# Optimization experiments

Measured on AMD Instinct MI355X. Metric: run time of the kernel, lower is better.

Reference implementation:

```python
import jax, jax.numpy as jnp
import numpy as np

H, DK, NHID, L, G = 8, 32, 256, 2, 16
SQRT_DK = float(np.sqrt(DK))
N_IN = (3, 3, 2)  # number of etypes whose dst is word, topic, doc (for mean cross-reducer)


def _seg_softmax_agg(a, val, dst, n):
    # per-destination-node softmax over incoming edges (DGL mailbox softmax), then weighted sum
    m = jax.ops.segment_max(a, dst, num_segments=n)
    m = jnp.where(m < -1e30, 0.0, m)  # empty segments
    ex = jnp.exp(a - m[dst])
    den = jax.ops.segment_sum(ex, dst, num_segments=n)
    w = ex / jnp.maximum(den, 1e-9)[dst]
    return jax.ops.segment_sum(w[..., None] * val, dst, num_segments=n)  # [n,H,DK]


def _forward(word_id, topic_id, g_word, g_topic, g_doc,
             src_ww, dst_ww, src_wd, dst_wd, src_wt, dst_wt, src_td, dst_td, src_tt, dst_tt,
             time_ww, time_wd, time_wt, time_td, y_data,
             word_embeds, topic_embeds, doc_gen, adapt_w, adapt_b,
             time_tab, time_w, time_b,
             kW, kB, qW, qB, vW, vB, aW, aB, skip, ln_g, ln_b,
             pri, attR, msgR, out_w, out_b):
    nd = g_doc.shape[0]
    # initial node features: word via adapt_ws, topic lookup, doc broadcast
    h = [word_embeds[word_id] @ adapt_w + adapt_b,
         topic_embeds[topic_id],
         jnp.tile(doc_gen, (nd, 1))]
    te = lambda t: time_tab[t] @ time_w + time_b  # RelTemporalEncoding: lin(emb(t)) -> [E, DK]
    th_ww, th_wd, th_wt, th_td = te(time_ww), te(time_wd), te(time_wt), te(time_td)
    # etype index order: wt, wd, td, tt, ww, tw, dt, dw ; ntype index: 0=word,1=topic,2=doc
    rels = [(0, 0, 1, src_wt, dst_wt, th_wt), (1, 0, 2, src_wd, dst_wd, th_wd),
            (2, 1, 2, src_td, dst_td, th_td), (3, 1, 1, src_tt, dst_tt, None),
            (4, 0, 0, src_ww, dst_ww, th_ww), (5, 1, 0, dst_wt, src_wt, th_wt),
            (6, 2, 1, dst_td, src_td, th_td), (7, 2, 0, dst_wd, src_wd, th_wd)]
    for li in range(L):
        k = [(h[i] @ kW[li, i] + kB[li, i]).reshape(-1, H, DK) for i in range(3)]
        q = [(h[i] @ qW[li, i] + qB[li, i]).reshape(-1, H, DK) for i in range(3)]
        v = [(h[i] @ vW[li, i] + vB[li, i]).reshape(-1, H, DK) for i in range(3)]
        t = [jnp.zeros((h[i].shape[0], NHID), h[i].dtype) for i in range(3)]
        for (e, s, d, src, dst, th) in rels:
            key = jnp.einsum('ehk,hkl->ehl', k[s][src], attR[li, e])
            a = (q[d][dst] * key).sum(-1) * pri[li, e] / SQRT_DK  # [E,H]
            val = jnp.einsum('ehk,hkl->ehl', v[s][src], msgR[li, e])
            if th is not None:
                val = val + th[:, None, :]  # temporal encoding broadcast over heads
            n = h[d].shape[0]
            he = _seg_softmax_agg(a, val, dst, n)
            t[d] = t[d] + jax.nn.relu(he.reshape(n, NHID))  # relu per etype, then mean
        nh = []
        for i in range(3):
            alpha = jax.nn.sigmoid(skip[li, i])
            trans = (t[i] / N_IN[i]) @ aW[li, i] + aB[li, i]
            out = trans * alpha + h[i] * (1.0 - alpha)
            mu = out.mean(-1, keepdims=True)
            var = ((out - mu) ** 2).mean(-1, keepdims=True)
            nh.append((out - mu) / jnp.sqrt(var + 1e-5) * ln_g[li, i] + ln_b[li, i])
        h = nh
    gmax = lambda x, g: jax.ops.segment_max(x, g, num_segments=G)  # dgl.max_nodes
    gi = jnp.concatenate([gmax(h[2], g_doc), gmax(h[0], g_word), gmax(h[1], g_topic)], -1)
    logits = gi @ out_w + out_b  # [G,1]
    z = logits.reshape(-1)
    loss = jnp.mean(jnp.maximum(z, 0.0) - z * y_data + jnp.log1p(jnp.exp(-jnp.abs(z))))
    return loss, jax.nn.sigmoid(logits)


def setup_inputs():
    key = jax.random.key(0)
    ks = iter(jax.random.split(key, 80))
    nrm = lambda shape, s=0.05: jax.random.normal(next(ks), shape, jnp.float32) * s
    ri = lambda shape, hi: jax.random.randint(next(ks), shape, 0, hi)
    NW, NT, ND = 30000, 2000, 8000
    d = {}
    d['word_id'] = ri((NW,), 15000)
    d['topic_id'] = ri((NT,), 50)
    d['g_word'] = jnp.sort(ri((NW,), G))
    d['g_topic'] = jnp.sort(ri((NT,), G))
    d['g_doc'] = jnp.sort(ri((ND,), G))
    d['src_ww'] = ri((40000,), NW); d['dst_ww'] = ri((40000,), NW); d['time_ww'] = ri((40000,), 7)
    d['src_wd'] = ri((30000,), NW); d['dst_wd'] = ri((30000,), ND); d['time_wd'] = ri((30000,), 7)
    d['src_wt'] = ri((30000,), NW); d['dst_wt'] = ri((30000,), NT); d['time_wt'] = ri((30000,), 7)
    d['src_td'] = ri((25000,), NT); d['dst_td'] = ri((25000,), ND); d['time_td'] = ri((25000,), 7)
    d['src_tt'] = ri((20000,), NT); d['dst_tt'] = ri((20000,), NT)
    d['y_data'] = jax.random.uniform(next(ks), (G,), jnp.float32)
    d['word_embeds'] = nrm((15000, 256))
    d['topic_embeds'] = nrm((50, 256), 0.1)
    d['doc_gen'] = nrm((1, 256), 0.1)
    d['adapt_w'] = nrm((256, 256)); d['adapt_b'] = nrm((256,), 0.01)
    d['time_tab'] = nrm((7, 32), 0.1); d['time_w'] = nrm((32, 32), 0.1); d['time_b'] = nrm((32,), 0.01)
    for nm in ['kW', 'qW', 'vW', 'aW']:
        d[nm] = nrm((L, 3, 256, 256))
    for nm in ['kB', 'qB', 'vB', 'aB']:
        d[nm] = nrm((L, 3, 256), 0.01)
    d['skip'] = jnp.ones((L, 3))
    d['ln_g'] = jnp.ones((L, 3, 256)); d['ln_b'] = jnp.zeros((L, 3, 256))
    d['pri'] = jnp.ones((L, 8, H))
    d['attR'] = nrm((L, 8, H, DK, DK), 0.1)
    d['msgR'] = nrm((L, 8, H, DK, DK), 0.1)
    d['out_w'] = nrm((3 * NHID, 1)); d['out_b'] = jnp.zeros((1,))
    return d


def reference(word_id, topic_id, g_word, g_topic, g_doc,
              src_ww, dst_ww, time_ww, src_wd, dst_wd, time_wd,
              src_wt, dst_wt, time_wt, src_td, dst_td, time_td,
              src_tt, dst_tt, y_data,
              word_embeds, topic_embeds, doc_gen, adapt_w, adapt_b,
              time_tab, time_w, time_b,
              kW, kB, qW, qB, vW, vB, aW, aB, skip, ln_g, ln_b,
              pri, attR, msgR, out_w, out_b):
    return _forward(word_id, topic_id, g_word, g_topic, g_doc,
                    src_ww, dst_ww, src_wd, dst_wd, src_wt, dst_wt, src_td, dst_td, src_tt, dst_tt,
                    time_ww, time_wd, time_wt, time_td, y_data,
                    word_embeds, topic_embeds, doc_gen, adapt_w, adapt_b,
                    time_tab, time_w, time_b,
                    kW, kB, qW, qB, vW, vB, aW, aB, skip, ln_g, ln_b,
                    pri, attR, msgR, out_w, out_b)
```

## Files before the change

kernel.cpp:

```cpp
#include <hip/hip_runtime.h>
#include <hip/hip_bf16.h>
#include <math.h>

#define H 8
#define DK 32
#define NHID 256
#define LNUM 2
#define GNUM 16

typedef float f32x4 __attribute__((ext_vector_type(4)));
typedef short bf16x8 __attribute__((ext_vector_type(8)));
typedef unsigned short u16x8 __attribute__((ext_vector_type(8)));

__device__ __forceinline__ unsigned encf(float f) {
    unsigned u = __float_as_uint(f);
    return (u & 0x80000000u) ? ~u : (u | 0x80000000u);
}
__device__ __forceinline__ float decf(unsigned u) {
    return __uint_as_float((u & 0x80000000u) ? (u ^ 0x80000000u) : ~u);
}
__device__ __forceinline__ float bfd(unsigned short u) {
    return __uint_as_float(((unsigned)u) << 16);
}
__device__ __forceinline__ unsigned short f2bf(float x) {
    __hip_bfloat16 b = __float2bfloat16(x);
    return *reinterpret_cast<unsigned short*>(&b);
}

#define APAN2(row, kb) ((((kb) >> 7) << 12) + ((row) << 6) + ((((kb) & 127) ^ (((row) & 7) << 4)) >> 1))
__device__ __forceinline__ size_t swzA(int row, int col ) {
    return (((size_t)(row >> 6)) << 14) + (size_t)APAN2(row & 63, col * 2);
}
#define SWZB(row, kb)  (((row) << 6) + ((((kb) ^ (((row) & 7) << 4))) >> 1))

struct CsrArgs { const int* dst[8]; int relOfs[9]; int dstBase[8]; };
struct BdArgs  { const unsigned short* inK[3]; const unsigned short* inV[3];
                 const float* RA[3]; const float* RM[3]; const float* priP[3];
                 int rows[3]; int rowOfs[3]; };
struct Ek1Args { const int* src[3]; const int* dst[3]; int E[3]; int eBase[3]; int rowOfs[3]; };
struct Ek3Args { const int* src[3]; const int* tim[3]; int eBase[3]; int dstBase[3];
                 int rowOfs[3]; int nr; int nD; };
struct GmaxArgs{ const float* hp[3]; const int* grp[3]; int n[3]; int colBase[3]; };
struct GBArgs  { int rb[4]; int nLoc[3]; int li3; };
struct MLArgs  { int rowOfs[4]; int nLoc[3]; int li3; };

__global__ void te_kernel(const float* __restrict__ time_tab, const float* __restrict__ time_w,
                          const float* __restrict__ time_b, float* __restrict__ te7) {
    int t = threadIdx.x >> 5, j = threadIdx.x & 31;
    if (t < 7) {
        float s = time_b[j];
        #pragma unroll
        for (int i = 0; i < 32; ++i) s += time_tab[t * 32 + i] * time_w[i * 32 + j];
        te7[t * 32 + j] = s;
    }
}

__global__ void gather_rows(const float* __restrict__ emb, const int* __restrict__ idx,
                            float* __restrict__ out, unsigned short* __restrict__ outB, int n) {
    int row = blockIdx.x, c = threadIdx.x;
    if (row < n) {
        float v = emb[(size_t)idx[row] * 256 + c];
        out[(size_t)row * 256 + c] = v;
        outB[swzA(row, c)] = f2bf(v);
    }
}

__global__ void bcast_row(const float* __restrict__ src, float* __restrict__ out,
                          unsigned short* __restrict__ outB, int n) {
    int row = blockIdx.x, c = threadIdx.x;
    if (row < n) {
        float v = src[c];
        out[(size_t)row * 256 + c] = v;
        outB[swzA(row, c)] = f2bf(v);
    }
}

__global__ __launch_bounds__(256) void wtr_kernel(
    const float* __restrict__ adaptW, const float* __restrict__ kW, const float* __restrict__ qW,
    const float* __restrict__ vW, const float* __restrict__ aW, unsigned short* __restrict__ WT) {
    int z = blockIdx.z;
    const float* src;
    if (z == 0) src = adaptW;
    else if (z < 7)  src = kW + (size_t)(z - 1) * 65536;
    else if (z < 13) src = qW + (size_t)(z - 7) * 65536;
    else if (z < 19) src = vW + (size_t)(z - 13) * 65536;
    else             src = aW + (size_t)(z - 19) * 65536;
    unsigned short* dst = WT + (size_t)z * 65536;
    __shared__ float tile[32][33];
    int tx = threadIdx.x & 31, ty = threadIdx.x >> 5;
    int kb = blockIdx.x * 32, cb = blockIdx.y * 32;
    #pragma unroll
    for (int i = 0; i < 4; ++i)
        tile[ty + i * 8][tx] = src[(size_t)(kb + ty + i * 8) * 256 + cb + tx];
    __syncthreads();
    #pragma unroll
    for (int i = 0; i < 4; ++i) {
        int col = cb + ty + i * 8, k = kb + tx;
        dst[((col >> 6) * 4 + (k >> 6)) * 4096 + SWZB(col & 63, (k & 63) * 2)] =
            f2bf(tile[tx][ty + i * 8]);
    }
}

__global__ __launch_bounds__(256) void gemm_batch(
    const unsigned short* __restrict__ Apan,
    const unsigned short* __restrict__ WT, int wBase, int nz,
    const float* __restrict__ b0, const float* __restrict__ b1, const float* __restrict__ b2,
    void* __restrict__ o0, void* __restrict__ o1, void* __restrict__ o2,
    int outBf16, GBArgs ga)
{
    __shared__ unsigned short As[64 * 256];
    __shared__ unsigned short Bs[2][4096];
    const int tid = threadIdx.x;
    const int lane = tid & 63, wv = tid >> 6;
    const int b = blockIdx.x;
    const int t = (b >= ga.rb[2]) ? 2 : ((b >= ga.rb[1]) ? 1 : 0);
    const int nLoc = ga.nLoc[t];
    const int locRowBase = (b - ga.rb[t]) * 64;
    const int cb6 = blockIdx.y;
    const int mBase = wBase + ga.li3 + t;
    {
        const u16x8* src = reinterpret_cast<const u16x8*>(Apan + (((size_t)b) << 14));
        u16x8* dst = reinterpret_cast<u16x8*>(As);
        #pragma unroll
        for (int it = 0; it < 8; ++it)
            dst[it * 256 + tid] = src[it * 256 + tid];
    }
    const int fr = lane & 15, fg = lane >> 4;
    const int wrow = (wv & 1) * 32, wcol = (wv >> 1) * 32;
    const int nt = nz * 4;
    {
        const u16x8* src = reinterpret_cast<const u16x8*>(WT + (size_t)mBase * 65536 + (size_t)(cb6 * 4 + 0) * 4096);
        u16x8* dst = reinterpret_cast<u16x8*>(Bs[0]);
        dst[tid] = src[tid];
        dst[tid + 256] = src[tid + 256];
    }
    __syncthreads();

    f32x4 acc[2][2];
    #pragma unroll
    for (int m = 0; m < 2; ++m)
        #pragma unroll
        for (int nn = 0; nn < 2; ++nn) acc[m][nn] = 0.f;

    for (int tt2 = 0; tt2 < nt; ++tt2) {
        const int cur = tt2 & 1;
        const int ks = tt2 & 3, z = tt2 >> 2;
        u16x8 w0, w1;
        const bool pf = (tt2 + 1 < nt);
        if (pf) {
            int tn = tt2 + 1;
            const u16x8* src = reinterpret_cast<const u16x8*>(
                WT + (size_t)(mBase + (tn >> 2) * 6) * 65536 + (size_t)(cb6 * 4 + (tn & 3)) * 4096);
            w0 = src[tid];
            w1 = src[tid + 256];
        }
        #pragma unroll
        for (int kk = 0; kk < 2; ++kk) {
            bf16x8 af0 = *reinterpret_cast<bf16x8*>(&As[APAN2(wrow + fr,      ks * 128 + kk * 64 + fg * 16)]);
            bf16x8 af1 = *reinterpret_cast<bf16x8*>(&As[APAN2(wrow + 16 + fr, ks * 128 + kk * 64 + fg * 16)]);
            bf16x8 bf0 = *reinterpret_cast<bf16x8*>(&Bs[cur][SWZB(wcol + fr,      kk * 64 + fg * 16)]);
            bf16x8 bf1 = *reinterpret_cast<bf16x8*>(&Bs[cur][SWZB(wcol + 16 + fr, kk * 64 + fg * 16)]);
            acc[0][0] = __builtin_amdgcn_mfma_f32_16x16x32_bf16(af0, bf0, acc[0][0], 0, 0, 0);
            acc[0][1] = __builtin_amdgcn_mfma_f32_16x16x32_bf16(af0, bf1, acc[0][1], 0, 0, 0);
            acc[1][0] = __builtin_amdgcn_mfma_f32_16x16x32_bf16(af1, bf0, acc[1][0], 0, 0, 0);
            acc[1][1] = __builtin_amdgcn_mfma_f32_16x16x32_bf16(af1, bf1, acc[1][1], 0, 0, 0);
        }
        if (pf) {
            u16x8* dst = reinterpret_cast<u16x8*>(Bs[cur ^ 1]);
            dst[tid] = w0;
            dst[tid + 256] = w1;
        }
        if (ks == 3) {
            const float* biasB = (z == 0) ? b0 : ((z == 1) ? b1 : b2);
            const float* bias = biasB + (size_t)(ga.li3 + t) * 256;
            void* outp = (z == 0) ? o0 : ((z == 1) ? o1 : o2);
            #pragma unroll
            for (int m = 0; m < 2; ++m) {
                #pragma unroll
                for (int r = 0; r < 4; ++r) {
                    int lr = locRowBase + wrow + m * 16 + fg * 4 + r;
                    if (lr >= nLoc) continue;
                    size_t gr = (size_t)b * 64 + wrow + m * 16 + fg * 4 + r;
                    #pragma unroll
                    for (int nn = 0; nn < 2; ++nn) {
                        int gc = cb6 * 64 + wcol + nn * 16 + fr;
                        float v = acc[m][nn][r] + bias[gc];
                        if (outBf16) ((unsigned short*)outp)[gr * 256 + gc] = f2bf(v);
                        else         ((float*)outp)[gr * 256 + gc] = v;
                    }
                }
            }
            #pragma unroll
            for (int m = 0; m < 2; ++m)
                #pragma unroll
                for (int nn = 0; nn < 2; ++nn) acc[m][nn] = 0.f;
        }
        __syncthreads();
    }
}

__global__ __launch_bounds__(256) void gemm_init(
    const float* __restrict__ A, const int* __restrict__ gidx,
    const unsigned short* __restrict__ WT, const float* __restrict__ bias,
    float* __restrict__ outF, unsigned short* __restrict__ dupB, int n)
{
    __shared__ unsigned short As[64 * 256];
    __shared__ unsigned short Bs[2][4096];
    const int tid = threadIdx.x;
    const int lane = tid & 63, wv = tid >> 6;
    const int rowBase = blockIdx.x * 64;
    const int cb6 = blockIdx.y;
    #pragma unroll 4
    for (int it = 0; it < 16; ++it) {
        int row = it * 4 + wv;
        int r = rowBase + row;
        ushort4 p = make_ushort4(0, 0, 0, 0);
        if (r < n) {
            int ar = gidx[r];
            float4 v = *reinterpret_cast<const float4*>(A + (size_t)ar * 256 + lane * 4);
            p.x = f2bf(v.x); p.y = f2bf(v.y); p.z = f2bf(v.z); p.w = f2bf(v.w);
        }
        *reinterpret_cast<ushort4*>(&As[APAN2(row, lane * 8)]) = p;
    }
    const int fr = lane & 15, fg = lane >> 4;
    const int wrow = (wv & 1) * 32, wcol = (wv >> 1) * 32;
    {
        const u16x8* src = reinterpret_cast<const u16x8*>(WT + (size_t)(cb6 * 4 + 0) * 4096);
        u16x8* dst = reinterpret_cast<u16x8*>(Bs[0]);
        dst[tid] = src[tid];
        dst[tid + 256] = src[tid + 256];
    }
    __syncthreads();
    f32x4 acc[2][2];
    #pragma unroll
    for (int m = 0; m < 2; ++m)
        #pragma unroll
        for (int nn = 0; nn < 2; ++nn) acc[m][nn] = 0.f;
    for (int t = 0; t < 4; ++t) {
        const int cur = t & 1;
        u16x8 w0, w1;
        const bool pf = (t + 1 < 4);
        if (pf) {
            const u16x8* src = reinterpret_cast<const u16x8*>(WT + (size_t)(cb6 * 4 + t + 1) * 4096);
            w0 = src[tid];
            w1 = src[tid + 256];
        }
        #pragma unroll
        for (int kk = 0; kk < 2; ++kk) {
            bf16x8 af0 = *reinterpret_cast<bf16x8*>(&As[APAN2(wrow + fr,      t * 128 + kk * 64 + fg * 16)]);
            bf16x8 af1 = *reinterpret_cast<bf16x8*>(&As[APAN2(wrow + 16 + fr, t * 128 + kk * 64 + fg * 16)]);
            bf16x8 bf0 = *reinterpret_cast<bf16x8*>(&Bs[cur][SWZB(wcol + fr,      kk * 64 + fg * 16)]);
            bf16x8 bf1 = *reinterpret_cast<bf16x8*>(&Bs[cur][SWZB(wcol + 16 + fr, kk * 64 + fg * 16)]);
            acc[0][0] = __builtin_amdgcn_mfma_f32_16x16x32_bf16(af0, bf0, acc[0][0], 0, 0, 0);
            acc[0][1] = __builtin_amdgcn_mfma_f32_16x16x32_bf16(af0, bf1, acc[0][1], 0, 0, 0);
            acc[1][0] = __builtin_amdgcn_mfma_f32_16x16x32_bf16(af1, bf0, acc[1][0], 0, 0, 0);
            acc[1][1] = __builtin_amdgcn_mfma_f32_16x16x32_bf16(af1, bf1, acc[1][1], 0, 0, 0);
        }
        if (pf) {
            u16x8* dst = reinterpret_cast<u16x8*>(Bs[cur ^ 1]);
            dst[tid] = w0;
            dst[tid + 256] = w1;
        }
        __syncthreads();
    }
    #pragma unroll
    for (int m = 0; m < 2; ++m) {
        #pragma unroll
        for (int r = 0; r < 4; ++r) {
            int gr = rowBase + wrow + m * 16 + fg * 4 + r;
            if (gr >= n) continue;
            #pragma unroll
            for (int nn = 0; nn < 2; ++nn) {
                int gc = cb6 * 64 + wcol + nn * 16 + fr;
                float v = acc[m][nn][r] + bias[gc];
                outF[(size_t)gr * 256 + gc] = v;
                dupB[swzA(gr, gc)] = f2bf(v);
            }
        }
    }
}

__global__ __launch_bounds__(256) void bd_mfma(
    unsigned short* __restrict__ katt, unsigned short* __restrict__ vmsg, BdArgs A)
{
    const int rr = blockIdx.z >> 1, isV = blockIdx.z & 1;
    const int n = A.rows[rr];
    const int rowBase = blockIdx.x * 128;
    if (rowBase >= n) return;
    const unsigned short* in = isV ? A.inV[rr] : A.inK[rr];
    const float* R = isV ? A.RM[rr] : A.RA[rr];
    unsigned short* out = (isV ? vmsg : katt) + (size_t)A.rowOfs[rr] * 256;
    const int head = blockIdx.y;
    const float oscale = isV ? 1.f : (A.priP[rr][head] * 0.17677669529663687f);
    const int tid = threadIdx.x, lane = tid & 63, wv = tid >> 6;
    const int fr = lane & 15, fg = lane >> 4;
    const float* Rh = R + head * 1024;
    bf16x8 b0, b1;
    #pragma unroll
    for (int j = 0; j < 8; ++j) {
        b0[j] = (short)f2bf(Rh[(fg * 8 + j) * 32 + fr] * oscale);
        b1[j] = (short)f2bf(Rh[(fg * 8 + j) * 32 + 16 + fr] * oscale);
    }
    const int r0 = rowBase + wv * 32 + fr;
    const int r1 = r0 + 16;
    const int rc0 = (r0 < n) ? r0 : n - 1;
    const int rc1 = (r1 < n) ? r1 : n - 1;
    bf16x8 a0 = *reinterpret_cast<const bf16x8*>(in + (size_t)rc0 * 256 + head * 32 + fg * 8);
    bf16x8 a1 = *reinterpret_cast<const bf16x8*>(in + (size_t)rc1 * 256 + head * 32 + fg * 8);
    f32x4 acc00 = 0.f, acc01 = 0.f, acc10 = 0.f, acc11 = 0.f;
    acc00 = __builtin_amdgcn_mfma_f32_16x16x32_bf16(a0, b0, acc00, 0, 0, 0);
    acc01 = __builtin_amdgcn_mfma_f32_16x16x32_bf16(a0, b1, acc01, 0, 0, 0);
    acc10 = __builtin_amdgcn_mfma_f32_16x16x32_bf16(a1, b0, acc10, 0, 0, 0);
    acc11 = __builtin_amdgcn_mfma_f32_16x16x32_bf16(a1, b1, acc11, 0, 0, 0);
    const int colB = head * 32 + fr;
    #pragma unroll
    for (int r = 0; r < 4; ++r) {
        int g0 = rowBase + wv * 32 + fg * 4 + r;
        if (g0 < n) {
            out[(size_t)g0 * 256 + colB]      = f2bf(acc00[r]);
            out[(size_t)g0 * 256 + colB + 16] = f2bf(acc01[r]);
        }
        int g1 = g0 + 16;
        if (g1 < n) {
            out[(size_t)g1 * 256 + colB]      = f2bf(acc10[r]);
            out[(size_t)g1 * 256 + colB + 16] = f2bf(acc11[r]);
        }
    }
}

__global__ __launch_bounds__(256) void ek1_group(
    const unsigned short* __restrict__ qbuf, const unsigned short* __restrict__ katt,
    float* __restrict__ alog, Ek1Args A)
{
    const int rr = blockIdx.y;
    int gid = blockIdx.x * 256 + threadIdx.x;
    int e = gid >> 3, h = gid & 7;
    if (e >= A.E[rr]) return;
    int s = A.src[rr][e], d = A.dst[rr][e];
    const u16x8* q8 = reinterpret_cast<const u16x8*>(qbuf + (size_t)d * 256 + h * 32);
    const u16x8* k8 = reinterpret_cast<const u16x8*>(katt + ((size_t)(A.rowOfs[rr] + s)) * 256 + h * 32);
    float a = 0.f;
    #pragma unroll
    for (int j = 0; j < 4; ++j) {
        u16x8 qv = q8[j], kv = k8[j];
        #pragma unroll
        for (int m = 0; m < 8; ++m) a += bfd(qv[m]) * bfd(kv[m]);
    }
    alog[(size_t)(A.eBase[rr] + e) * 8 + h] = a;
}

__global__ __launch_bounds__(256) void ek3_group(
    const unsigned short* __restrict__ vmsg, const float* __restrict__ alog,
    const int* __restrict__ rowptrAll, const int* __restrict__ eidxAll,
    const float* __restrict__ te7, unsigned short* __restrict__ tacc, float outScale, Ek3Args A)
{
    __shared__ float sTe[224];
    if (threadIdx.x < 224) sTe[threadIdx.x] = te7[threadIdx.x];
    __syncthreads();
    int wv = threadIdx.x >> 6, lane = threadIdx.x & 63;
    int d = blockIdx.x * 4 + wv;
    if (d >= A.nD) return;
    const int bl = lane >> 3, hl = lane & 7;
    const int c = lane * 4, hq = lane >> 3;
    float t0 = 0.f, t1 = 0.f, t2 = 0.f, t3 = 0.f;
    for (int rr = 0; rr < A.nr; ++rr) {
        int base = A.dstBase[rr] + d;
        int beg = rowptrAll[base], end = rowptrAll[base + 1];
        if (beg == end) continue;
        const int* srcp = A.src[rr];
        const int* timp = A.tim[rr];
        int eB = A.eBase[rr], rO = A.rowOfs[rr];
        float m = -INFINITY, den = 0.f;
        float a0 = 0.f, a1 = 0.f, a2 = 0.f, a3 = 0.f;
        for (int p0 = beg; p0 < end; p0 += 8) {
            int p = p0 + bl;
            bool valid = p < end;
            int ge = eidxAll[valid ? p : end - 1];
            int le = ge - eB;
            float a = valid ? alog[(size_t)ge * 8 + hl] : -INFINITY;
            int sS = valid ? srcp[le] : 0;
            int tT = (timp && valid) ? timp[le] : 0;
            float bm = a;
            bm = fmaxf(bm, __shfl_xor(bm, 8));
            bm = fmaxf(bm, __shfl_xor(bm, 16));
            bm = fmaxf(bm, __shfl_xor(bm, 32));
            float bmA = __shfl(bm, hq);
            float mN = fmaxf(m, bmA);
            float sc = __expf(m - mN);
            den *= sc; a0 *= sc; a1 *= sc; a2 *= sc; a3 *= sc;
            m = mN;
            float mL = __shfl(mN, hl * 8);
            float ex = valid ? __expf(a - mL) : 0.f;
            float ds = ex;
            ds += __shfl_xor(ds, 8);
            ds += __shfl_xor(ds, 16);
            ds += __shfl_xor(ds, 32);
            den += __shfl(ds, hq);
            int nb = end - p0; if (nb > 8) nb = 8;
            for (int b = 0; b < nb; ++b) {
                float w = __shfl(ex, b * 8 + hq);
                int sB = __shfl(sS, b * 8);
                ushort4 v = *reinterpret_cast<const ushort4*>(vmsg + ((size_t)(rO + sB)) * 256 + c);
                float vx = bfd(v.x), vy = bfd(v.y), vz = bfd(v.z), vw = bfd(v.w);
                if (timp) {
                    int tB = __shfl(tT, b * 8);
                    const float* tp = &sTe[tB * 32 + (c & 31)];
                    vx += tp[0]; vy += tp[1]; vz += tp[2]; vw += tp[3];
                }
                a0 += w * vx; a1 += w * vy; a2 += w * vz; a3 += w * vw;
            }
        }
        float inv = 1.f / fmaxf(den, 1e-9f);
        t0 += fmaxf(a0 * inv, 0.f); t1 += fmaxf(a1 * inv, 0.f);
        t2 += fmaxf(a2 * inv, 0.f); t3 += fmaxf(a3 * inv, 0.f);
    }
    ushort4 o;
    o.x = f2bf(t0 * outScale); o.y = f2bf(t1 * outScale);
    o.z = f2bf(t2 * outScale); o.w = f2bf(t3 * outScale);
    *reinterpret_cast<ushort4*>(tacc + swzA(d, c)) = o;
}

__global__ void count_all(CsrArgs A, int* __restrict__ cnt, int totE) {
    int gid = blockIdx.x * 256 + threadIdx.x;
    if (gid >= totE) return;
    int r = 0;
    while (gid >= A.relOfs[r + 1]) ++r;
    int e = gid - A.relOfs[r];
    atomicAdd(&cnt[A.dstBase[r] + A.dst[r][e]], 1);
}
__global__ __launch_bounds__(1024) void scan1_k(const int* __restrict__ cnt, int* __restrict__ part,
                                                int* __restrict__ bsum, int n) {
    __shared__ int buf[1024];
    int tid = threadIdx.x, gid = blockIdx.x * 1024 + tid;
    int x = (gid < n) ? cnt[gid] : 0;
    buf[tid] = x; __syncthreads();
    for (int off = 1; off < 1024; off <<= 1) {
        int y = (tid >= off) ? buf[tid - off] : 0;
        __syncthreads();
        buf[tid] += y;
        __syncthreads();
    }
    if (gid < n) part[gid] = buf[tid];
    if (tid == 1023) bsum[blockIdx.x] = buf[1023];
}
__global__ __launch_bounds__(256) void scan2_k(int* __restrict__ bsum, int nb) {
    __shared__ int buf[256];
    int tid = threadIdx.x;
    buf[tid] = (tid < nb) ? bsum[tid] : 0;
    __syncthreads();
    for (int off = 1; off < 256; off <<= 1) {
        int y = (tid >= off) ? buf[tid - off] : 0;
        __syncthreads();
        buf[tid] += y;
        __syncthreads();
    }
    if (tid < nb) bsum[tid] = buf[tid];
}
__global__ void scan3_k(const int* __restrict__ cnt, const int* __restrict__ part,
                        const int* __restrict__ bsum, int* __restrict__ rowptr,
                        int* __restrict__ cur, int n) {
    int gid = blockIdx.x * 256 + threadIdx.x;
    if (gid < n) {
        int b = gid >> 10;
        int add = (b > 0) ? bsum[b - 1] : 0;
        int inc = part[gid] + add;
        rowptr[gid + 1] = inc;
        cur[gid] = inc - cnt[gid];
    }
    if (gid == 0) rowptr[0] = 0;
}
__global__ void scatter_all(CsrArgs A, int* __restrict__ cur, int* __restrict__ eidx, int totE) {
    int gid = blockIdx.x * 256 + threadIdx.x;
    if (gid >= totE) return;
    int r = 0;
    while (gid >= A.relOfs[r + 1]) ++r;
    int e = gid - A.relOfs[r];
    int p = atomicAdd(&cur[A.dstBase[r] + A.dst[r][e]], 1);
    eidx[p] = gid;
}

__global__ __launch_bounds__(256) void mix_ln_all(
    float* __restrict__ h, unsigned short* __restrict__ hB, const float* __restrict__ trans,
    const float* __restrict__ skipP, const float* __restrict__ g, const float* __restrict__ b,
    MLArgs M)
{
    int row = blockIdx.x;
    int t = (row >= M.rowOfs[2]) ? 2 : ((row >= M.rowOfs[1]) ? 1 : 0);
    int d = row - M.rowOfs[t];
    if (d >= M.nLoc[t]) return;
    int j = M.li3 + t;
    int c = threadIdx.x;
    float alpha = 1.f / (1.f + expf(-skipP[j]));
    size_t off = (size_t)row * 256 + c;
    float o = trans[off] * alpha + h[off] * (1.f - alpha);
    float s = o, ss = o * o;
    #pragma unroll
    for (int dd = 1; dd < 64; dd <<= 1) { s += __shfl_xor(s, dd); ss += __shfl_xor(ss, dd); }
    __shared__ float rS[4], rSS[4];
    int w = threadIdx.x >> 6, lane = threadIdx.x & 63;
    if (lane == 0) { rS[w] = s; rSS[w] = ss; }
    __syncthreads();
    float S = rS[0] + rS[1] + rS[2] + rS[3];
    float SS = rSS[0] + rSS[1] + rSS[2] + rSS[3];
    float mean = S * (1.f / 256.f);
    float var = fmaxf(SS * (1.f / 256.f) - mean * mean, 0.f);
    float rs = rsqrtf(var + 1e-5f);
    float v = (o - mean) * rs * g[(size_t)j * 256 + c] + b[(size_t)j * 256 + c];
    h[off] = v;
    hB[swzA(row, c)] = f2bf(v);
}

__global__ __launch_bounds__(256) void gmax_all(GmaxArgs A, unsigned* __restrict__ gi) {
    int ty = blockIdx.y;
    int n = A.n[ty];
    int r0 = blockIdx.x * 64;
    if (r0 >= n) return;
    int col = threadIdx.x;
    const float* hp = A.hp[ty];
    const int* grp = A.grp[ty];
    int cbase = A.colBase[ty];
    int rend = (r0 + 64 < n) ? r0 + 64 : n;
    int cur = grp[r0];
    float m = -INFINITY;
    for (int r = r0; r < rend; ++r) {
        int g = grp[r];
        if (g != cur) {
            atomicMax(&gi[cur * 768 + cbase + col], encf(m));
            cur = g; m = -INFINITY;
        }
        m = fmaxf(m, hp[(size_t)r * 256 + col]);
    }
    atomicMax(&gi[cur * 768 + cbase + col], encf(m));
}

__global__ void gi_init(unsigned* __restrict__ gi) {
    int i = blockIdx.x * 256 + threadIdx.x;
    if (i < 16 * 768) gi[i] = 0x007FFFFFu;
}

__global__ __launch_bounds__(1024) void final_k(const unsigned* __restrict__ gi,
                                                const float* __restrict__ out_w,
                                                const float* __restrict__ out_b,
                                                const float* __restrict__ y,
                                                float* __restrict__ out) {
    int w = threadIdx.x >> 6, lane = threadIdx.x & 63;
    float s = 0.f;
    for (int c = lane; c < 768; c += 64) s += decf(gi[w * 768 + c]) * out_w[c];
    #pragma unroll
    for (int d = 1; d < 64; d <<= 1) s += __shfl_xor(s, d);
    __shared__ float lloss[16];
    if (lane == 0) {
        float z = s + out_b[0];
        out[1 + w] = 1.f / (1.f + expf(-z));
        lloss[w] = fmaxf(z, 0.f) - z * y[w] + log1pf(expf(-fabsf(z)));
    }
    __syncthreads();
    if (threadIdx.x == 0) {
        float L = 0.f;
        for (int g2 = 0; g2 < 16; ++g2) L += lloss[g2];
        out[0] = L * (1.f / 16.f);
    }
}

extern "C" void kernel_launch(void* const* d_in, const int* in_sizes, int n_in,
                              void* d_out, int out_size, void* d_ws, size_t ws_size,
                              hipStream_t stream) {
    const int* word_id   = (const int*)d_in[0];
    const int* topic_id  = (const int*)d_in[1];
    const int* g_word    = (const int*)d_in[2];
    const int* g_topic   = (const int*)d_in[3];
    const int* g_doc     = (const int*)d_in[4];
    const int* src_ww = (const int*)d_in[5];  const int* dst_ww = (const int*)d_in[6];  const int* time_ww = (const int*)d_in[7];
    const int* src_wd = (const int*)d_in[8];  const int* dst_wd = (const int*)d_in[9];  const int* time_wd = (const int*)d_in[10];
    const int* src_wt = (const int*)d_in[11]; const int* dst_wt = (const int*)d_in[12]; const int* time_wt = (const int*)d_in[13];
    const int* src_td = (const int*)d_in[14]; const int* dst_td = (const int*)d_in[15]; const int* time_td = (const int*)d_in[16];
    const int* src_tt = (const int*)d_in[17]; const int* dst_tt = (const int*)d_in[18];
    const float* y_data      = (const float*)d_in[19];
    const float* word_embeds = (const float*)d_in[20];
    const float* topic_embeds= (const float*)d_in[21];
    const float* doc_gen     = (const float*)d_in[22];
    const float* adapt_w     = (const float*)d_in[23];
    const float* adapt_b     = (const float*)d_in[24];
    const float* time_tab    = (const float*)d_in[25];
    const float* time_w      = (const float*)d_in[26];
    const float* time_b      = (const float*)d_in[27];
    const float* kW = (const float*)d_in[28];
    const float* qW = (const float*)d_in[29];
    const float* vW = (const float*)d_in[30];
    const float* aW = (const float*)d_in[31];
    const float* kB = (const float*)d_in[32];
    const float* qB = (const float*)d_in[33];
    const float* vB = (const float*)d_in[34];
    const float* aB = (const float*)d_in[35];
    const float* skip = (const float*)d_in[36];
    const float* ln_g = (const float*)d_in[37];
    const float* ln_b = (const float*)d_in[38];
    const float* pri  = (const float*)d_in[39];
    const float* attR = (const float*)d_in[40];
    const float* msgR = (const float*)d_in[41];
    const float* out_w = (const float*)d_in[42];
    const float* out_b = (const float*)d_in[43];

    const int NW = in_sizes[0], NT = in_sizes[1], ND = in_sizes[4];
    const int E_ww = in_sizes[5], E_wd = in_sizes[8], E_wt = in_sizes[11],
              E_td = in_sizes[14], E_tt = in_sizes[17];
    const int nN[3] = {NW, NT, ND};
    const float invNin[3] = {1.f / 3.f, 1.f / 3.f, 1.f / 2.f};

    struct Rel { int e, s, d; const int* src; const int* dst; const int* tim; int E; };
    const Rel rels[8] = {
        {0, 0, 1, src_wt, dst_wt, time_wt, E_wt},
        {1, 0, 2, src_wd, dst_wd, time_wd, E_wd},
        {2, 1, 2, src_td, dst_td, time_td, E_td},
        {3, 1, 1, src_tt, dst_tt, nullptr, E_tt},
        {4, 0, 0, src_ww, dst_ww, time_ww, E_ww},
        {5, 1, 0, dst_wt, src_wt, time_wt, E_wt},
        {6, 2, 1, dst_td, src_td, time_td, E_td},
        {7, 2, 0, dst_wd, src_wd, time_wd, E_wd},
    };

    int relOfs[9]; relOfs[0] = 0;
    int dstBase[8]; int acc = 0;
    for (int r = 0; r < 8; ++r) { relOfs[r + 1] = relOfs[r] + rels[r].E; dstBase[r] = acc; acc += nN[rels[r].d]; }
    const int totE = relOfs[8], totD = acc;

    const int grpRels[3][3] = {{4, 5, 7}, {0, 3, 6}, {1, 2, 0}};
    const int nrG[3] = {3, 3, 2};
    int rowOfsG[3][3], grpRows[3];
    for (int g = 0; g < 3; ++g) {
        int ro = 0;
        for (int j = 0; j < nrG[g]; ++j) { rowOfsG[g][j] = ro; ro += nN[rels[grpRels[g][j]].s]; }
        grpRows[g] = ro;
    }
    int maxGrpRows = 0;
    for (int g = 0; g < 3; ++g) if (grpRows[g] > maxGrpRows) maxGrpRows = grpRows[g];

    int nPad[3], rowOfsT[4];
    rowOfsT[0] = 0;
    for (int i = 0; i < 3; ++i) { nPad[i] = (nN[i] + 63) & ~63; rowOfsT[i + 1] = rowOfsT[i] + nPad[i]; }
    const int totPad = rowOfsT[3];

    float* base = (float*)d_ws;
    size_t off = 0;
    auto take = [&](size_t nElems) { float* p = base + off; off += (nElems + 63) & ~(size_t)63; return p; };
    float* hPbase = take((size_t)totPad * 256);
    unsigned short* hB = (unsigned short*)take((size_t)totPad * 128);
    unsigned short* tB = (unsigned short*)take((size_t)totPad * 128);
    unsigned short* kPb = (unsigned short*)take((size_t)totPad * 128);
    unsigned short* qPb = (unsigned short*)take((size_t)totPad * 128);
    unsigned short* vPb = (unsigned short*)take((size_t)totPad * 128);
    size_t uniFloats = (size_t)maxGrpRows * 256;
    if ((size_t)totPad * 256 > uniFloats) uniFloats = (size_t)totPad * 256;
    float* uni = take(uniFloats);
    unsigned short* kattB = (unsigned short*)uni;
    unsigned short* vmsgB = (unsigned short*)(uni + (size_t)maxGrpRows * 128);
    float* trans = uni;
    unsigned short* WT = (unsigned short*)take((size_t)25 * 32768);
    float* alog = take((size_t)totE * 8);
    float* te7  = take(7 * 32);
    unsigned* gi = (unsigned*)take(16 * 768);
    int* cntAll = (int*)take(totD);
    int* part   = (int*)take(totD);
    int* bsum   = (int*)take(256);
    int* rowptrAll = (int*)take(totD + 1);
    int* curAll = (int*)take(totD);
    int* eidxAll = (int*)take(totE);
    (void)ws_size; (void)n_in; (void)out_size;

    te_kernel<<<1, 256, 0, stream>>>(time_tab, time_w, time_b, te7);
    {
        dim3 g(8, 8, 25);
        wtr_kernel<<<g, 256, 0, stream>>>(adapt_w, kW, qW, vW, aW, WT);
    }
    CsrArgs ca;
    for (int r = 0; r < 8; ++r) { ca.dst[r] = rels[r].dst; ca.dstBase[r] = dstBase[r]; }
    for (int r = 0; r < 9; ++r) ca.relOfs[r] = relOfs[r];
    hipMemsetAsync(cntAll, 0, (size_t)totD * sizeof(int), stream);
    count_all<<<(totE + 255) / 256, 256, 0, stream>>>(ca, cntAll, totE);
    int nb = (totD + 1023) / 1024;
    scan1_k<<<nb, 1024, 0, stream>>>(cntAll, part, bsum, totD);
    scan2_k<<<1, 256, 0, stream>>>(bsum, nb);
    scan3_k<<<(totD + 255) / 256, 256, 0, stream>>>(cntAll, part, bsum, rowptrAll, curAll, totD);
    scatter_all<<<(totE + 255) / 256, 256, 0, stream>>>(ca, curAll, eidxAll, totE);
    gi_init<<<48, 256, 0, stream>>>(gi);

    {
        dim3 g((NW + 63) / 64, 4);
        gemm_init<<<g, 256, 0, stream>>>(word_embeds, word_id, WT, adapt_b, hPbase, hB, NW);
    }
    gather_rows<<<NT, 256, 0, stream>>>(topic_embeds, topic_id,
                                        hPbase + (size_t)rowOfsT[1] * 256,
                                        hB + (size_t)rowOfsT[1] * 256, NT);
    bcast_row<<<ND, 256, 0, stream>>>(doc_gen,
                                      hPbase + (size_t)rowOfsT[2] * 256,
                                      hB + (size_t)rowOfsT[2] * 256, ND);

    Ek1Args e1a[3]; Ek3Args e3a[3];
    int maxE_g[3];
    for (int g = 0; g < 3; ++g) {
        int me = 0;
        for (int j = 0; j < 3; ++j) {
            int jr = (j < nrG[g]) ? grpRels[g][j] : grpRels[g][0];
            const Rel& R = rels[jr];
            e1a[g].src[j] = R.src; e1a[g].dst[j] = R.dst;
            e1a[g].E[j] = (j < nrG[g]) ? R.E : 0;
            e1a[g].eBase[j] = relOfs[jr];
            e1a[g].rowOfs[j] = (j < nrG[g]) ? rowOfsG[g][j] : 0;
            e3a[g].src[j] = R.src; e3a[g].tim[j] = R.tim;
            e3a[g].eBase[j] = relOfs[jr]; e3a[g].dstBase[j] = dstBase[jr];
            e3a[g].rowOfs[j] = (j < nrG[g]) ? rowOfsG[g][j] : 0;
            if (j < nrG[g] && R.E > me) me = R.E;
        }
        e3a[g].nr = nrG[g]; e3a[g].nD = nN[g];
        maxE_g[g] = me;
    }

    GBArgs gb;
    for (int i = 0; i < 4; ++i) gb.rb[i] = rowOfsT[i] / 64;
    for (int i = 0; i < 3; ++i) gb.nLoc[i] = nN[i];
    MLArgs ml;
    for (int i = 0; i < 4; ++i) ml.rowOfs[i] = rowOfsT[i];
    for (int i = 0; i < 3; ++i) ml.nLoc[i] = nN[i];

    const int totBlocks = totPad / 64;
    for (int li = 0; li < LNUM; ++li) {
        gb.li3 = li * 3; ml.li3 = li * 3;
        {
            dim3 g(totBlocks, 4);
            gemm_batch<<<g, 256, 0, stream>>>(hB, WT, 1, 3, kB, qB, vB,
                                              kPb, qPb, vPb, 1, gb);
        }
        for (int g = 0; g < 3; ++g) {
            BdArgs ba;
            int maxRows = 0;
            for (int j = 0; j < 3; ++j) {
                int jr = (j < nrG[g]) ? grpRels[g][j] : grpRels[g][0];
                const Rel& R = rels[jr];
                ba.inK[j] = kPb + (size_t)rowOfsT[R.s] * 256;
                ba.inV[j] = vPb + (size_t)rowOfsT[R.s] * 256;
                ba.RA[j] = attR + ((size_t)li * 8 + R.e) * 8192;
                ba.RM[j] = msgR + ((size_t)li * 8 + R.e) * 8192;
                ba.priP[j] = pri + ((size_t)li * 8 + R.e) * 8;
                ba.rows[j] = (j < nrG[g]) ? nN[R.s] : 0;
                ba.rowOfs[j] = (j < nrG[g]) ? rowOfsG[g][j] : 0;
                if (ba.rows[j] > maxRows) maxRows = ba.rows[j];
            }
            dim3 gbd((maxRows + 127) / 128, 8, 2 * nrG[g]);
            bd_mfma<<<gbd, 256, 0, stream>>>(kattB, vmsgB, ba);
            dim3 g1((maxE_g[g] * 8 + 255) / 256, nrG[g]);
            ek1_group<<<g1, 256, 0, stream>>>(qPb + (size_t)rowOfsT[g] * 256, kattB, alog, e1a[g]);
            ek3_group<<<(nN[g] + 3) / 4, 256, 0, stream>>>(vmsgB, alog, rowptrAll, eidxAll,
                                                           te7, tB + (size_t)rowOfsT[g] * 256,
                                                           invNin[g], e3a[g]);
        }
        {
            dim3 g(totBlocks, 4);
            gemm_batch<<<g, 256, 0, stream>>>(tB, WT, 19, 1, aB, aB, aB,
                                              trans, trans, trans, 0, gb);
        }
        mix_ln_all<<<totPad, 256, 0, stream>>>(hPbase, hB, trans, skip, ln_g, ln_b, ml);
    }

    GmaxArgs ga;
    ga.hp[0] = hPbase + (size_t)rowOfsT[2] * 256; ga.grp[0] = g_doc;   ga.n[0] = ND; ga.colBase[0] = 0;
    ga.hp[1] = hPbase;                             ga.grp[1] = g_word;  ga.n[1] = NW; ga.colBase[1] = 256;
    ga.hp[2] = hPbase + (size_t)rowOfsT[1] * 256; ga.grp[2] = g_topic; ga.n[2] = NT; ga.colBase[2] = 512;
    int maxN = NW > ND ? (NW > NT ? NW : NT) : (ND > NT ? ND : NT);
    dim3 gg((maxN + 63) / 64, 3);
    gmax_all<<<gg, 256, 0, stream>>>(ga, gi);
    final_k<<<1, 1024, 0, stream>>>(gi, out_w, out_b, y_data, (float*)d_out);
}
```

Before: 717.0 us.

## Batch all relations into single bd/ek1/ek3 launches per layer

Replaces the per-destination-type loop of three kernel groups with whole-layer launches covering all eight relations: one bd for keys, one ek1 for logits, one bd for messages reusing the same arena, and one ek3 over all destination nodes. This cuts kernel launches and serialization between small groups and gives each launch a larger grid. In exchange the arena is sized for every relation's rows, and ek3 picks its type by branching on a global node index, which can leave work unevenly spread across blocks.

```diff
diff --git a/kernel.cpp b/kernel.cpp
--- a/kernel.cpp
+++ b/kernel.cpp
@@ -33,16 +33,16 @@
 }
 #define SWZB(row, kb)  (((row) << 6) + ((((kb) ^ (((row) & 7) << 4))) >> 1))
 
-struct CsrArgs { const int* dst[8]; int relOfs[9]; int dstBase[8]; };
-struct BdArgs  { const unsigned short* inK[3]; const unsigned short* inV[3];
-                 const float* RA[3]; const float* RM[3]; const float* priP[3];
-                 int rows[3]; int rowOfs[3]; };
-struct Ek1Args { const int* src[3]; const int* dst[3]; int E[3]; int eBase[3]; int rowOfs[3]; };
-struct Ek3Args { const int* src[3]; const int* tim[3]; int eBase[3]; int dstBase[3];
-                 int rowOfs[3]; int nr; int nD; };
-struct GmaxArgs{ const float* hp[3]; const int* grp[3]; int n[3]; int colBase[3]; };
-struct GBArgs  { int rb[4]; int nLoc[3]; int li3; };
-struct MLArgs  { int rowOfs[4]; int nLoc[3]; int li3; };
+struct CsrArgs  { const int* dst[8]; int relOfs[9]; int dstBase[8]; };
+struct BdAllArgs{ int rows[8]; int srcOfs[8]; int outOfs[8]; };
+struct Ek1AllArgs{ const int* src[8]; const int* dst[8]; int E[8]; int eBase[8];
+                   int kOfs[8]; int qOfs[8]; };
+struct Ek3AllArgs{ const int* src[8]; const int* tim[8]; int eBase[8]; int dstBase[8];
+                   int vOfs[8]; int typeRel[9]; int nrT[3]; int cumN[4]; int tOfs[3];
+                   float oScale[3]; };
+struct GmaxArgs { const float* hp[3]; const int* grp[3]; int n[3]; int colBase[3]; };
+struct GBArgs   { int rb[4]; int nLoc[3]; int li3; };
+struct MLArgs   { int rowOfs[4]; int nLoc[3]; int li3; };
 
 __global__ void te_kernel(const float* __restrict__ time_tab, const float* __restrict__ time_w,
                           const float* __restrict__ time_b, float* __restrict__ te7) {
@@ -280,18 +280,20 @@
     }
 }
 
-__global__ __launch_bounds__(256) void bd_mfma(
-    unsigned short* __restrict__ katt, unsigned short* __restrict__ vmsg, BdArgs A)
+__global__ __launch_bounds__(256) void bd_all(
+    const unsigned short* __restrict__ inPb, const float* __restrict__ Rl,
+    const float* __restrict__ priL, int isV,
+    unsigned short* __restrict__ outAll, BdAllArgs A)
 {
-    const int rr = blockIdx.z >> 1, isV = blockIdx.z & 1;
-    const int n = A.rows[rr];
+    const int rel = blockIdx.z;
+    const int n = A.rows[rel];
     const int rowBase = blockIdx.x * 128;
     if (rowBase >= n) return;
-    const unsigned short* in = isV ? A.inV[rr] : A.inK[rr];
-    const float* R = isV ? A.RM[rr] : A.RA[rr];
-    unsigned short* out = (isV ? vmsg : katt) + (size_t)A.rowOfs[rr] * 256;
+    const unsigned short* in = inPb + (size_t)A.srcOfs[rel] * 256;
+    const float* R = Rl + (size_t)rel * 8192;
+    unsigned short* out = outAll + (size_t)A.outOfs[rel] * 256;
     const int head = blockIdx.y;
-    const float oscale = isV ? 1.f : (A.priP[rr][head] * 0.17677669529663687f);
+    const float oscale = isV ? 1.f : (priL[rel * 8 + head] * 0.17677669529663687f);
     const int tid = threadIdx.x, lane = tid & 63, wv = tid >> 6;
     const int fr = lane & 15, fg = lane >> 4;
     const float* Rh = R + head * 1024;
@@ -328,17 +330,17 @@
     }
 }
 
-__global__ __launch_bounds__(256) void ek1_group(
-    const unsigned short* __restrict__ qbuf, const unsigned short* __restrict__ katt,
-    float* __restrict__ alog, Ek1Args A)
+__global__ __launch_bounds__(256) void ek1_all(
+    const unsigned short* __restrict__ qPb, const unsigned short* __restrict__ kattAll,
+    float* __restrict__ alog, Ek1AllArgs A)
 {
-    const int rr = blockIdx.y;
+    const int rel = blockIdx.y;
     int gid = blockIdx.x * 256 + threadIdx.x;
     int e = gid >> 3, h = gid & 7;
-    if (e >= A.E[rr]) return;
-    int s = A.src[rr][e], d = A.dst[rr][e];
-    const u16x8* q8 = reinterpret_cast<const u16x8*>(qbuf + (size_t)d * 256 + h * 32);
-    const u16x8* k8 = reinterpret_cast<const u16x8*>(katt + ((size_t)(A.rowOfs[rr] + s)) * 256 + h * 32);
+    if (e >= A.E[rel]) return;
+    int s = A.src[rel][e], d = A.dst[rel][e];
+    const u16x8* q8 = reinterpret_cast<const u16x8*>(qPb + ((size_t)(A.qOfs[rel] + d)) * 256 + h * 32);
+    const u16x8* k8 = reinterpret_cast<const u16x8*>(kattAll + ((size_t)(A.kOfs[rel] + s)) * 256 + h * 32);
     float a = 0.f;
     #pragma unroll
     for (int j = 0; j < 4; ++j) {
@@ -346,30 +348,34 @@
         #pragma unroll
         for (int m = 0; m < 8; ++m) a += bfd(qv[m]) * bfd(kv[m]);
     }
-    alog[(size_t)(A.eBase[rr] + e) * 8 + h] = a;
-}
-
-__global__ __launch_bounds__(256) void ek3_group(
-    const unsigned short* __restrict__ vmsg, const float* __restrict__ alog,
+    alog[(size_t)(A.eBase[rel] + e) * 8 + h] = a;
+}
+
+__global__ __launch_bounds__(256) void ek3_all(
+    const unsigned short* __restrict__ vmsgAll, const float* __restrict__ alog,
     const int* __restrict__ rowptrAll, const int* __restrict__ eidxAll,
-    const float* __restrict__ te7, unsigned short* __restrict__ tacc, float outScale, Ek3Args A)
+    const float* __restrict__ te7, unsigned short* __restrict__ tB, Ek3AllArgs A)
 {
     __shared__ float sTe[224];
     if (threadIdx.x < 224) sTe[threadIdx.x] = te7[threadIdx.x];
     __syncthreads();
     int wv = threadIdx.x >> 6, lane = threadIdx.x & 63;
-    int d = blockIdx.x * 4 + wv;
-    if (d >= A.nD) return;
+    int dg = blockIdx.x * 4 + wv;
+    if (dg >= A.cumN[3]) return;
+    const int ty = (dg >= A.cumN[2]) ? 2 : ((dg >= A.cumN[1]) ? 1 : 0);
+    const int d = dg - A.cumN[ty];
     const int bl = lane >> 3, hl = lane & 7;
     const int c = lane * 4, hq = lane >> 3;
     float t0 = 0.f, t1 = 0.f, t2 = 0.f, t3 = 0.f;
-    for (int rr = 0; rr < A.nr; ++rr) {
-        int base = A.dstBase[rr] + d;
+    const int nr = A.nrT[ty];
+    for (int j = 0; j < nr; ++j) {
+        const int rel = A.typeRel[ty * 3 + j];
+        int base = A.dstBase[rel] + d;
         int beg = rowptrAll[base], end = rowptrAll[base + 1];
         if (beg == end) continue;
-        const int* srcp = A.src[rr];
-        const int* timp = A.tim[rr];
-        int eB = A.eBase[rr], rO = A.rowOfs[rr];
+        const int* srcp = A.src[rel];
+        const int* timp = A.tim[rel];
+        int eB = A.eBase[rel], rO = A.vOfs[rel];
         float m = -INFINITY, den = 0.f;
         float a0 = 0.f, a1 = 0.f, a2 = 0.f, a3 = 0.f;
         for (int p0 = beg; p0 < end; p0 += 8) {
@@ -400,11 +406,11 @@
             for (int b = 0; b < nb; ++b) {
                 float w = __shfl(ex, b * 8 + hq);
                 int sB = __shfl(sS, b * 8);
-                ushort4 v = *reinterpret_cast<const ushort4*>(vmsg + ((size_t)(rO + sB)) * 256 + c);
+                ushort4 v = *reinterpret_cast<const ushort4*>(vmsgAll + ((size_t)(rO + sB)) * 256 + c);
                 float vx = bfd(v.x), vy = bfd(v.y), vz = bfd(v.z), vw = bfd(v.w);
                 if (timp) {
-                    int tB = __shfl(tT, b * 8);
-                    const float* tp = &sTe[tB * 32 + (c & 31)];
+                    int tBt = __shfl(tT, b * 8);
+                    const float* tp = &sTe[tBt * 32 + (c & 31)];
                     vx += tp[0]; vy += tp[1]; vz += tp[2]; vw += tp[3];
                 }
                 a0 += w * vx; a1 += w * vy; a2 += w * vz; a3 += w * vw;
@@ -414,10 +420,11 @@
         t0 += fmaxf(a0 * inv, 0.f); t1 += fmaxf(a1 * inv, 0.f);
         t2 += fmaxf(a2 * inv, 0.f); t3 += fmaxf(a3 * inv, 0.f);
     }
+    float os = A.oScale[ty];
     ushort4 o;
-    o.x = f2bf(t0 * outScale); o.y = f2bf(t1 * outScale);
-    o.z = f2bf(t2 * outScale); o.w = f2bf(t3 * outScale);
-    *reinterpret_cast<ushort4*>(tacc + swzA(d, c)) = o;
+    o.x = f2bf(t0 * os); o.y = f2bf(t1 * os);
+    o.z = f2bf(t2 * os); o.w = f2bf(t3 * os);
+    *reinterpret_cast<ushort4*>(tB + swzA(A.tOfs[ty] + d, c)) = o;
 }
 
 __global__ void count_all(CsrArgs A, int* __restrict__ cnt, int totE) {
@@ -624,16 +631,13 @@
     for (int r = 0; r < 8; ++r) { relOfs[r + 1] = relOfs[r] + rels[r].E; dstBase[r] = acc; acc += nN[rels[r].d]; }
     const int totE = relOfs[8], totD = acc;
 
-    const int grpRels[3][3] = {{4, 5, 7}, {0, 3, 6}, {1, 2, 0}};
-    const int nrG[3] = {3, 3, 2};
-    int rowOfsG[3][3], grpRows[3];
-    for (int g = 0; g < 3; ++g) {
-        int ro = 0;
-        for (int j = 0; j < nrG[g]; ++j) { rowOfsG[g][j] = ro; ro += nN[rels[grpRels[g][j]].s]; }
-        grpRows[g] = ro;
-    }
-    int maxGrpRows = 0;
-    for (int g = 0; g < 3; ++g) if (grpRows[g] > maxGrpRows) maxGrpRows = grpRows[g];
+    int relRowOfs[8], relRowsTot = 0, maxRelRows = 0, maxE = 0;
+    for (int r = 0; r < 8; ++r) {
+        relRowOfs[r] = relRowsTot;
+        relRowsTot += nN[rels[r].s];
+        if (nN[rels[r].s] > maxRelRows) maxRelRows = nN[rels[r].s];
+        if (rels[r].E > maxE) maxE = rels[r].E;
+    }
 
     int nPad[3], rowOfsT[4];
     rowOfsT[0] = 0;
@@ -649,11 +653,10 @@
     unsigned short* kPb = (unsigned short*)take((size_t)totPad * 128);
     unsigned short* qPb = (unsigned short*)take((size_t)totPad * 128);
     unsigned short* vPb = (unsigned short*)take((size_t)totPad * 128);
-    size_t uniFloats = (size_t)maxGrpRows * 256;
-    if ((size_t)totPad * 256 > uniFloats) uniFloats = (size_t)totPad * 256;
-    float* uni = take(uniFloats);
-    unsigned short* kattB = (unsigned short*)uni;
-    unsigned short* vmsgB = (unsigned short*)(uni + (size_t)maxGrpRows * 128);
+    size_t arenaFloats = (size_t)relRowsTot * 128;
+    if ((size_t)totPad * 256 > arenaFloats) arenaFloats = (size_t)totPad * 256;
+    float* uni = take(arenaFloats);
+    unsigned short* arena = (unsigned short*)uni;
     float* trans = uni;
     unsigned short* WT = (unsigned short*)take((size_t)25 * 32768);
     float* alog = take((size_t)totE * 8);
@@ -695,25 +698,24 @@
                                       hPbase + (size_t)rowOfsT[2] * 256,
                                       hB + (size_t)rowOfsT[2] * 256, ND);
 
-    Ek1Args e1a[3]; Ek3Args e3a[3];
-    int maxE_g[3];
-    for (int g = 0; g < 3; ++g) {
-        int me = 0;
-        for (int j = 0; j < 3; ++j) {
-            int jr = (j < nrG[g]) ? grpRels[g][j] : grpRels[g][0];
-            const Rel& R = rels[jr];
-            e1a[g].src[j] = R.src; e1a[g].dst[j] = R.dst;
-            e1a[g].E[j] = (j < nrG[g]) ? R.E : 0;
-            e1a[g].eBase[j] = relOfs[jr];
-            e1a[g].rowOfs[j] = (j < nrG[g]) ? rowOfsG[g][j] : 0;
-            e3a[g].src[j] = R.src; e3a[g].tim[j] = R.tim;
-            e3a[g].eBase[j] = relOfs[jr]; e3a[g].dstBase[j] = dstBase[jr];
-            e3a[g].rowOfs[j] = (j < nrG[g]) ? rowOfsG[g][j] : 0;
-            if (j < nrG[g] && R.E > me) me = R.E;
-        }
-        e3a[g].nr = nrG[g]; e3a[g].nD = nN[g];
-        maxE_g[g] = me;
-    }
+    BdAllArgs ba;
+    Ek1AllArgs e1;
+    Ek3AllArgs e3;
+    for (int r = 0; r < 8; ++r) {
+        const Rel& R = rels[r];
+        ba.rows[r] = nN[R.s];
+        ba.srcOfs[r] = rowOfsT[R.s];
+        ba.outOfs[r] = relRowOfs[r];
+        e1.src[r] = R.src; e1.dst[r] = R.dst; e1.E[r] = R.E; e1.eBase[r] = relOfs[r];
+        e1.kOfs[r] = relRowOfs[r]; e1.qOfs[r] = rowOfsT[R.d];
+        e3.src[r] = R.src; e3.tim[r] = R.tim; e3.eBase[r] = relOfs[r];
+        e3.dstBase[r] = dstBase[r]; e3.vOfs[r] = relRowOfs[r];
+    }
+    const int typeRel[9] = {4, 5, 7, 0, 3, 6, 1, 2, 0};
+    for (int i = 0; i < 9; ++i) e3.typeRel[i] = typeRel[i];
+    e3.nrT[0] = 3; e3.nrT[1] = 3; e3.nrT[2] = 2;
+    e3.cumN[0] = 0; e3.cumN[1] = NW; e3.cumN[2] = NW + NT; e3.cumN[3] = NW + NT + ND;
+    for (int i = 0; i < 3; ++i) { e3.tOfs[i] = rowOfsT[i]; e3.oScale[i] = invNin[i]; }
 
     GBArgs gb;
     for (int i = 0; i < 4; ++i) gb.rb[i] = rowOfsT[i] / 64;
@@ -723,6 +725,7 @@
     for (int i = 0; i < 3; ++i) ml.nLoc[i] = nN[i];
 
     const int totBlocks = totPad / 64;
+    const int totD3 = NW + NT + ND;
     for (int li = 0; li < LNUM; ++li) {
         gb.li3 = li * 3; ml.li3 = li * 3;
         {
@@ -730,29 +733,22 @@
             gemm_batch<<<g, 256, 0, stream>>>(hB, WT, 1, 3, kB, qB, vB,
                                               kPb, qPb, vPb, 1, gb);
         }
-        for (int g = 0; g < 3; ++g) {
-            BdArgs ba;
-            int maxRows = 0;
-            for (int j = 0; j < 3; ++j) {
-                int jr = (j < nrG[g]) ? grpRels[g][j] : grpRels[g][0];
-                const Rel& R = rels[jr];
-                ba.inK[j] = kPb + (size_t)rowOfsT[R.s] * 256;
-                ba.inV[j] = vPb + (size_t)rowOfsT[R.s] * 256;
-                ba.RA[j] = attR + ((size_t)li * 8 + R.e) * 8192;
-                ba.RM[j] = msgR + ((size_t)li * 8 + R.e) * 8192;
-                ba.priP[j] = pri + ((size_t)li * 8 + R.e) * 8;
-                ba.rows[j] = (j < nrG[g]) ? nN[R.s] : 0;
-                ba.rowOfs[j] = (j < nrG[g]) ? rowOfsG[g][j] : 0;
-                if (ba.rows[j] > maxRows) maxRows = ba.rows[j];
-            }
-            dim3 gbd((maxRows + 127) / 128, 8, 2 * nrG[g]);
-            bd_mfma<<<gbd, 256, 0, stream>>>(kattB, vmsgB, ba);
-            dim3 g1((maxE_g[g] * 8 + 255) / 256, nrG[g]);
-            ek1_group<<<g1, 256, 0, stream>>>(qPb + (size_t)rowOfsT[g] * 256, kattB, alog, e1a[g]);
-            ek3_group<<<(nN[g] + 3) / 4, 256, 0, stream>>>(vmsgB, alog, rowptrAll, eidxAll,
-                                                           te7, tB + (size_t)rowOfsT[g] * 256,
-                                                           invNin[g], e3a[g]);
-        }
+        {
+            dim3 g((maxRelRows + 127) / 128, 8, 8);
+            bd_all<<<g, 256, 0, stream>>>(kPb, attR + (size_t)li * 8 * 8192,
+                                          pri + (size_t)li * 8 * 8, 0, arena, ba);
+        }
+        {
+            dim3 g((maxE * 8 + 255) / 256, 8);
+            ek1_all<<<g, 256, 0, stream>>>(qPb, arena, alog, e1);
+        }
+        {
+            dim3 g((maxRelRows + 127) / 128, 8, 8);
+            bd_all<<<g, 256, 0, stream>>>(vPb, msgR + (size_t)li * 8 * 8192,
+                                          pri + (size_t)li * 8 * 8, 1, arena, ba);
+        }
+        ek3_all<<<(totD3 + 3) / 4, 256, 0, stream>>>(arena, alog, rowptrAll, eidxAll,
+                                                     te7, tB, e3);
         {
             dim3 g(totBlocks, 4);
             gemm_batch<<<g, 256, 0, stream>>>(tB, WT, 19, 1, aB, aB, aB,
```

Result: faster. 676.4 us (-5.7%).
